# Kernel optimization log

Hardware: AMD Instinct MI355X
Metric: run time of the kernel (lower is better)

The kernel has to match this reference:

```python
import jax, jax.numpy as jnp
import numpy as np

DIMS = [1024, 2048, 2048, 51]
B, P = 16, 1024


def setup_inputs() -> dict:
    key = jax.random.key(0)
    ks = jax.random.split(key, 1 + 2 * (len(DIMS) - 1))
    inp = {
        "num_pairs": P,
        "classifier_input": jax.random.normal(ks[0], (B, P, DIMS[0]), dtype=jnp.float32),
        "num_batches": B,
    }
    # Linear params, PyTorch-style: W[out, in], b[out]
    for li in range(len(DIMS) - 1):
        fan_in = DIMS[li]
        bound = 1.0 / np.sqrt(fan_in)
        inp[f"W{li}"] = jax.random.uniform(ks[1 + 2 * li], (DIMS[li + 1], fan_in), minval=-bound, maxval=bound, dtype=jnp.float32)
        inp[f"b{li}"] = jax.random.uniform(ks[2 + 2 * li], (DIMS[li + 1],), minval=-bound, maxval=bound, dtype=jnp.float32)
    return inp


def reference(num_pairs, classifier_input, num_batches, W0, b0, W1, b1, W2, b2):
    # Batched MLP over all (num_batches * num_pairs) vectors at once.
    # Original loops per (b, i); math is identical. dropout p=0.0 -> identity.
    x = classifier_input  # [B, P, d_in]
    x = jax.nn.relu(jnp.einsum("bpd,hd->bph", x, W0) + b0)
    x = jax.nn.relu(jnp.einsum("bpd,hd->bph", x, W1) + b1)
    out = jnp.einsum("bpd,od->bpo", x, W2) + b2  # [B, P, n_classes]
    return out
```

## Files before the change

### kernel.cpp

```cpp
#include <hip/hip_runtime.h>
#include <hip/hip_bf16.h>
#include <stdint.h>

typedef __attribute__((ext_vector_type(8))) short short8;
typedef __attribute__((ext_vector_type(8))) uint16_t ushort8;
typedef __attribute__((ext_vector_type(4))) float floatx4;

#define TK 64


__device__ __forceinline__ uint16_t f2bf_bits(float f) {
    uint32_t u = __builtin_bit_cast(uint32_t, f);
    u += 0x7FFFu + ((u >> 16) & 1u);
    return (uint16_t)(u >> 16);
}

__device__ __forceinline__ void async_copy16(const void* g, void* l) {
    auto gp = (const __attribute__((address_space(1))) uint32_t*)(uintptr_t)g;
    auto lp = (__attribute__((address_space(3))) uint32_t*)(uint32_t)(uintptr_t)l;
    __builtin_amdgcn_global_load_lds(gp, lp, 16, 0, 0);
}


__global__ void cvt8(const float* __restrict__ src, uint16_t* __restrict__ dst, int n) {
    int i = (blockIdx.x * 256 + threadIdx.x) * 8;
    if (i >= n) return;
    floatx4 a = *(const floatx4*)(src + i);
    floatx4 b = *(const floatx4*)(src + i + 4);
    ushort8 o;
#pragma unroll
    for (int k = 0; k < 4; k++) {
        o[k]     = f2bf_bits(a[k]);
        o[k + 4] = f2bf_bits(b[k]);
    }
    *(ushort8*)(dst + i) = o;
}

__global__ void cvt_pad_w2(const float* __restrict__ src, uint16_t* __restrict__ dst) {
    int i = (blockIdx.x * 256 + threadIdx.x) * 8;
    int row = i >> 11;
    ushort8 o;
    if (row < 51) {
        floatx4 a = *(const floatx4*)(src + i);
        floatx4 b = *(const floatx4*)(src + i + 4);
#pragma unroll
        for (int k = 0; k < 4; k++) {
            o[k]     = f2bf_bits(a[k]);
            o[k + 4] = f2bf_bits(b[k]);
        }
    } else {
#pragma unroll
        for (int k = 0; k < 8; k++) o[k] = 0;
    }
    *(ushort8*)(dst + i) = o;
}


template <int MI, int NJ, bool RELU, bool OUTF32>
__global__ __launch_bounds__(256, 2)
void gemm_bt(const uint16_t* __restrict__ A,
             const uint16_t* __restrict__ W,
             const float* __restrict__ bias,
             void* __restrict__ out,
             int M, int N, int K, int ldc, int nstore)
{
    constexpr int TMv = MI * 32;
    constexpr int TNv = NJ * 32;
    constexpr int ACH = TMv / 32;
    constexpr int BCH = TNv / 32;

    __shared__ alignas(16) uint16_t sA[TMv * TK];
    __shared__ alignas(16) uint16_t sB[TNv * TK];

    const int tid  = threadIdx.x;
    const int wave = tid >> 6;
    const int lane = tid & 63;

    const int f   = blockIdx.x;
    const int xcd = f & 7;
    const int loc = f >> 3;
    const int per = (int)gridDim.x >> 3;
    const int nt  = N / TNv;
    const int n_t = loc % nt;
    const int m_t = xcd * (per / nt) + loc / nt;
    const int n0 = n_t * TNv;
    const int m0 = m_t * TMv;

    floatx4 acc[MI][NJ];
    const floatx4 zero = {0.f, 0.f, 0.f, 0.f};
#pragma unroll
    for (int i = 0; i < MI; i++)
#pragma unroll
        for (int j = 0; j < NJ; j++) acc[i][j] = zero;

    const int wr = (wave >> 1) * MI * 16;
    const int wc = (wave & 1) * NJ * 16;

    const int sr   = lane >> 3;
    const int scol = ((lane & 7) ^ sr) * 8;

    const uint16_t* ap[ACH];
    const uint16_t* bp[BCH];
#pragma unroll
    for (int t = 0; t < ACH; t++)
        ap[t] = A + (size_t)(m0 + (wave + 4 * t) * 8 + sr) * K + scol;
#pragma unroll
    for (int t = 0; t < BCH; t++)
        bp[t] = W + (size_t)(n0 + (wave + 4 * t) * 8 + sr) * K + scol;

    const int fm = lane & 15;
    const int fr = fm & 7;
    const int kgb = lane >> 4;

    const int niter = K / TK;
    for (int it = 0; it < niter; it++) {
#pragma unroll
        for (int t = 0; t < ACH; t++) {
            async_copy16(ap[t], sA + (wave + 4 * t) * 512);
            ap[t] += TK;
        }
#pragma unroll
        for (int t = 0; t < BCH; t++) {
            async_copy16(bp[t], sB + (wave + 4 * t) * 512);
            bp[t] += TK;
        }
        __syncthreads();

#pragma unroll
        for (int kk = 0; kk < 2; kk++) {
            const int slot = ((kgb + 4 * kk) ^ fr) * 8;
            short8 af[MI], bfr[NJ];
#pragma unroll
            for (int i = 0; i < MI; i++)
                af[i] = *(const short8*)(sA + (wr + i * 16 + fm) * TK + slot);
#pragma unroll
            for (int j = 0; j < NJ; j++)
                bfr[j] = *(const short8*)(sB + (wc + j * 16 + fm) * TK + slot);
#pragma unroll
            for (int i = 0; i < MI; i++)
#pragma unroll
                for (int j = 0; j < NJ; j++)
                    acc[i][j] = __builtin_amdgcn_mfma_f32_16x16x32_bf16(af[i], bfr[j], acc[i][j], 0, 0, 0);
        }
        __syncthreads();
    }

    const int cr = (lane >> 4) * 4;
    const int cc = lane & 15;
#pragma unroll
    for (int i = 0; i < MI; i++) {
        const int gmb = m0 + wr + i * 16 + cr;
#pragma unroll
        for (int j = 0; j < NJ; j++) {
            const int gn = n0 + wc + j * 16 + cc;
            if (gn < nstore) {
                const float bv = bias[gn];
#pragma unroll
                for (int r = 0; r < 4; r++) {
                    float v = acc[i][j][r] + bv;
                    if (RELU) v = fmaxf(v, 0.f);
                    const size_t idx = (size_t)(gmb + r) * ldc + gn;
                    if (OUTF32) ((float*)out)[idx] = v;
                    else        ((uint16_t*)out)[idx] = f2bf_bits(v);
                }
            }
        }
    }
}


#define SCHED0 __builtin_amdgcn_sched_barrier(0)

#define LOAD_AF(SA, QM, DST) do { \
    const uint16_t* _p = (SA) + (QM) * 8192 + aoff; \
    _Pragma("unroll") \
    for (int kk = 0; kk < 2; kk++) { \
      const int sl = ((kgb + 4 * kk) ^ fr) * 8; \
      _Pragma("unroll") \
      for (int mi = 0; mi < 4; mi++) \
        DST[mi][kk] = *(const short8*)(_p + mi * 1024 + sl); \
    } } while (0)

#define LOAD_BF(SB, QN, BF) do { \
    const uint16_t* _p = (SB) + (QN) * 8192 + boff; \
    _Pragma("unroll") \
    for (int kk = 0; kk < 2; kk++) { \
      const int sl = ((kgb + 4 * kk) ^ fr) * 8; \
      _Pragma("unroll") \
      for (int nj = 0; nj < 2; nj++) \
        BF[nj][kk] = *(const short8*)(_p + nj * 1024 + sl); \
    } } while (0)

#define PH_SYNC \
    SCHED0; \
    asm volatile("s_waitcnt lgkmcnt(0)" ::: "memory"); \
    SCHED0; \
    __builtin_amdgcn_s_barrier(); \
    SCHED0;

#define PH_SYNC_VM \
    SCHED0; \
    asm volatile("s_waitcnt vmcnt(0) lgkmcnt(0)" ::: "memory"); \
    SCHED0; \
    __builtin_amdgcn_s_barrier(); \
    SCHED0;

#define MFMA_CL(QM, QN, AF, BF) \
    __builtin_amdgcn_s_setprio(1); \
    _Pragma("unroll") \
    for (int kk = 0; kk < 2; kk++) \
      _Pragma("unroll") \
      for (int mi = 0; mi < 4; mi++) \
        _Pragma("unroll") \
        for (int nj = 0; nj < 2; nj++) \
          acc[QM][QN][mi][nj] = __builtin_amdgcn_mfma_f32_16x16x32_bf16( \
              AF[mi][kk], BF[nj][kk], acc[QM][QN][mi][nj], 0, 0, 0); \
    __builtin_amdgcn_s_setprio(0); \
    SCHED0;

#define TILE_BODY(SAc, SBc, SAo, SBo, TT, STG) \
     \
    if (STG) { stB((TT) + 1, SBo); stA((TT) + 1, SAo); } \
    LOAD_AF(SAc, 0, af); \
    LOAD_BF(SBc, 0, b0); \
    LOAD_BF(SBc, 1, b1); \
    PH_SYNC; \
    MFMA_CL(0, 0, af, b0); \
    MFMA_CL(0, 1, af, b1); \
     \
    LOAD_AF(SAc, 1, af); \
    PH_SYNC_VM; \
    MFMA_CL(1, 0, af, b0); \
    MFMA_CL(1, 1, af, b1);

template <bool RELU, bool OUTF32>
__global__ __launch_bounds__(512, 2)
void gemm256(const uint16_t* __restrict__ A,
             const uint16_t* __restrict__ W,
             const float* __restrict__ bias,
             void* __restrict__ out,
             int K, int N, int ldc, int nstore)
{
    extern __shared__ uint16_t smem[];
    uint16_t* sA0 = smem;
    uint16_t* sA1 = smem + 16384;
    uint16_t* sB0 = smem + 32768;
    uint16_t* sB1 = smem + 49152;

    const int tid  = threadIdx.x;
    const int wave = tid >> 6;
    const int lane = tid & 63;
    const int wm2  = wave >> 2;
    const int wn2  = wave & 3;

    const int f   = blockIdx.x;
    const int xcd = f & 7;
    const int loc = f >> 3;
    const int per = (int)gridDim.x >> 3;
    const int ntn = N / 256;
    const int n_t = loc % ntn;
    const int m_t = xcd * (per / ntn) + loc / ntn;
    const int m0 = m_t * 256;
    const int n0 = n_t * 256;

    floatx4 acc[2][2][4][2];
    const floatx4 zero = {0.f, 0.f, 0.f, 0.f};
#pragma unroll
    for (int qm = 0; qm < 2; qm++)
#pragma unroll
    for (int qn = 0; qn < 2; qn++)
#pragma unroll
    for (int mi = 0; mi < 4; mi++)
#pragma unroll
    for (int nj = 0; nj < 2; nj++) acc[qm][qn][mi][nj] = zero;

    const int srow = lane >> 3;
    const int scol = ((lane & 7) ^ srow) * 8;
    const uint16_t* pA = A + (size_t)(m0 + wave * 8 + srow) * K + scol;
    const uint16_t* pB = W + (size_t)(n0 + wave * 8 + srow) * K + scol;

    auto stA = [&](int kt, uint16_t* buf) {
        const uint16_t* p = pA + (size_t)kt * 64;
        async_copy16(p,                    buf + wave * 512);
        async_copy16(p + (size_t)64  * K,  buf + 4096  + wave * 512);
        async_copy16(p + (size_t)128 * K,  buf + 8192  + wave * 512);
        async_copy16(p + (size_t)192 * K,  buf + 12288 + wave * 512);
    };
    auto stB = [&](int kt, uint16_t* buf) {
        const uint16_t* p = pB + (size_t)kt * 64;
        async_copy16(p,                    buf + wave * 512);
        async_copy16(p + (size_t)64  * K,  buf + 4096  + wave * 512);
        async_copy16(p + (size_t)128 * K,  buf + 8192  + wave * 512);
        async_copy16(p + (size_t)192 * K,  buf + 12288 + wave * 512);
    };

    const int fm  = lane & 15;
    const int fr  = fm & 7;
    const int kgb = lane >> 4;
    const int aoff = (wm2 * 64 + fm) * 64;
    const int boff = (wn2 * 32 + fm) * 64;

    short8 af[4][2];
    short8 b0[2][2];
    short8 b1[2][2];

    stB(0, sB0);
    stA(0, sA0);
    asm volatile("s_waitcnt vmcnt(0)" ::: "memory");
    __builtin_amdgcn_s_barrier();
    SCHED0;

    const int niter = K / 64;
    for (int it = 0; it < niter / 2 - 1; ++it) {
        TILE_BODY(sA0, sB0, sA1, sB1, 2 * it,     true);
        TILE_BODY(sA1, sB1, sA0, sB0, 2 * it + 1, true);
    }
    TILE_BODY(sA0, sB0, sA1, sB1, niter - 2, true);
    TILE_BODY(sA1, sB1, sA0, sB0, niter - 1, false);

    const int cr = (lane >> 4) * 4;
    const int cc = lane & 15;
#pragma unroll
    for (int qm = 0; qm < 2; qm++)
#pragma unroll
    for (int mi = 0; mi < 4; mi++) {
        const int gm = m0 + qm * 128 + wm2 * 64 + mi * 16 + cr;
#pragma unroll
        for (int qn = 0; qn < 2; qn++)
#pragma unroll
        for (int nj = 0; nj < 2; nj++) {
            const int gn = n0 + qn * 128 + wn2 * 32 + nj * 16 + cc;
            if (gn < nstore) {
                const float bv = bias[gn];
#pragma unroll
                for (int r = 0; r < 4; r++) {
                    float v = acc[qm][qn][mi][nj][r] + bv;
                    if (RELU) v = fmaxf(v, 0.f);
                    const size_t idx = (size_t)(gm + r) * ldc + gn;
                    if (OUTF32) ((float*)out)[idx] = v;
                    else        ((uint16_t*)out)[idx] = f2bf_bits(v);
                }
            }
        }
    }
}


extern "C" void kernel_launch(void* const* d_in, const int* in_sizes, int n_in,
                              void* d_out, int out_size, void* d_ws, size_t ws_size,
                              hipStream_t stream) {
    (void)in_sizes; (void)n_in; (void)out_size; (void)ws_size;
    const float* X  = (const float*)d_in[1];
    const float* W0 = (const float*)d_in[3];
    const float* b0 = (const float*)d_in[4];
    const float* W1 = (const float*)d_in[5];
    const float* b1 = (const float*)d_in[6];
    const float* W2 = (const float*)d_in[7];
    const float* b2 = (const float*)d_in[8];

    const int M = 16384;

    static bool attr_done = false;
    if (!attr_done) {
        (void)hipFuncSetAttribute((const void*)gemm256<true, false>,
                                  hipFuncAttributeMaxDynamicSharedMemorySize, 131072);
        attr_done = true;
    }

    char* w = (char*)d_ws;
    uint16_t* X0  = (uint16_t*)w; w += (size_t)M * 1024 * 2;
    uint16_t* X1  = (uint16_t*)w; w += (size_t)M * 2048 * 2;
    uint16_t* X2  = (uint16_t*)w; w += (size_t)M * 2048 * 2;
    uint16_t* W0b = (uint16_t*)w; w += (size_t)2048 * 1024 * 2;
    uint16_t* W1b = (uint16_t*)w; w += (size_t)2048 * 2048 * 2;
    uint16_t* W2b = (uint16_t*)w; w += (size_t)64 * 2048 * 2;

    cvt8<<<M * 1024 / 8 / 256, 256, 0, stream>>>(X, X0, M * 1024);
    cvt8<<<2048 * 1024 / 8 / 256, 256, 0, stream>>>(W0, W0b, 2048 * 1024);
    cvt8<<<2048 * 2048 / 8 / 256, 256, 0, stream>>>(W1, W1b, 2048 * 2048);
    cvt_pad_w2<<<64 * 2048 / 8 / 256, 256, 0, stream>>>(W2, W2b);

    gemm256<true, false><<<dim3((M / 256) * (2048 / 256)), 512, 131072, stream>>>(
        X0, W0b, b0, X1, 1024, 2048, 2048, 2048);
    gemm256<true, false><<<dim3((M / 256) * (2048 / 256)), 512, 131072, stream>>>(
        X1, W1b, b1, X2, 2048, 2048, 2048, 2048);
    gemm_bt<1, 2, false, true><<<dim3(M / 32), 256, 0, stream>>>(
        X2, W2b, b2, d_out, M, 64, 2048, 51, 51);
}
```

Baseline: 351.0 us.

## Restructure GEMM barrier schedule and add direct-load small-N final layer kernel

The main 256x256 GEMM loop changes its synchronisation: each phase now issues a barrier before waiting on LDS reads and adds trailing barriers, and the global-load wait moves to the end of the second half-window, so the LDS reads overlap the barrier. The final 51-column layer now uses a new kernel that loads A and W fragments straight from global memory into MFMA registers without LDS staging, replacing the tiled gemm_bt. This trades the LDS tiling for fewer instructions and no block-level syncs in the small-N layer, but it relies on the cache for reuse. The extra barriers in the main loop may also add stall time.

```diff
diff --git a/kernel.cpp b/kernel.cpp
--- a/kernel.cpp
+++ b/kernel.cpp
@@ -169,7 +169,70 @@
 }
 
 
+template <bool RELU, bool OUTF32>
+__global__ __launch_bounds__(256)
+void gemm_small_n(const uint16_t* __restrict__ A,
+                  const uint16_t* __restrict__ W,
+                  const float* __restrict__ bias,
+                  void* __restrict__ out,
+                  int K, int ldc, int nstore)
+{
+    const int tid  = threadIdx.x;
+    const int wave = tid >> 6;
+    const int lane = tid & 63;
+    const int wr = (wave >> 1) * 16;
+    const int wc = (wave & 1) * 32;
+
+    const int m0 = blockIdx.x * 32;
+    const int fm  = lane & 15;
+    const int kgb = lane >> 4;
+
+    const uint16_t* pa  = A + (size_t)(m0 + wr + fm) * K + kgb * 8;
+    const uint16_t* pb0 = W + (size_t)(wc + fm) * K + kgb * 8;
+    const uint16_t* pb1 = W + (size_t)(wc + 16 + fm) * K + kgb * 8;
+
+    floatx4 acc0 = {0.f, 0.f, 0.f, 0.f};
+    floatx4 acc1 = {0.f, 0.f, 0.f, 0.f};
+
+#pragma unroll 8
+    for (int k0 = 0; k0 < K; k0 += 64) {
+#pragma unroll
+        for (int kk = 0; kk < 2; kk++) {
+            const int off = k0 + kk * 32;
+            short8 a  = *(const short8*)(pa  + off);
+            short8 b0 = *(const short8*)(pb0 + off);
+            short8 b1 = *(const short8*)(pb1 + off);
+            acc0 = __builtin_amdgcn_mfma_f32_16x16x32_bf16(a, b0, acc0, 0, 0, 0);
+            acc1 = __builtin_amdgcn_mfma_f32_16x16x32_bf16(a, b1, acc1, 0, 0, 0);
+        }
+    }
+
+    const int cr = (lane >> 4) * 4;
+    const int cc = lane & 15;
+    const int gm = m0 + wr + cr;
+#pragma unroll
+    for (int j = 0; j < 2; j++) {
+        const int gn = wc + j * 16 + cc;
+        if (gn < nstore) {
+            const float bv = bias[gn];
+            const floatx4 av = j ? acc1 : acc0;
+#pragma unroll
+            for (int r = 0; r < 4; r++) {
+                float v = av[r] + bv;
+                if (RELU) v = fmaxf(v, 0.f);
+                const size_t idx = (size_t)(gm + r) * ldc + gn;
+                if (OUTF32) ((float*)out)[idx] = v;
+                else        ((uint16_t*)out)[idx] = f2bf_bits(v);
+            }
+        }
+    }
+}
+
+
 #define SCHED0 __builtin_amdgcn_sched_barrier(0)
+#define BAR    __builtin_amdgcn_s_barrier()
+#define LGKM0  asm volatile("s_waitcnt lgkmcnt(0)" ::: "memory")
+#define VM0    asm volatile("s_waitcnt vmcnt(0)" ::: "memory")
 
 #define LOAD_AF(SA, QM, DST) do { \
     const uint16_t* _p = (SA) + (QM) * 8192 + aoff; \
@@ -190,20 +253,6 @@
       for (int nj = 0; nj < 2; nj++) \
         BF[nj][kk] = *(const short8*)(_p + nj * 1024 + sl); \
     } } while (0)
-
-#define PH_SYNC \
-    SCHED0; \
-    asm volatile("s_waitcnt lgkmcnt(0)" ::: "memory"); \
-    SCHED0; \
-    __builtin_amdgcn_s_barrier(); \
-    SCHED0;
-
-#define PH_SYNC_VM \
-    SCHED0; \
-    asm volatile("s_waitcnt vmcnt(0) lgkmcnt(0)" ::: "memory"); \
-    SCHED0; \
-    __builtin_amdgcn_s_barrier(); \
-    SCHED0;
 
 #define MFMA_CL(QM, QN, AF, BF) \
     __builtin_amdgcn_s_setprio(1); \
@@ -218,20 +267,24 @@
     __builtin_amdgcn_s_setprio(0); \
     SCHED0;
 
-#define TILE_BODY(SAc, SBc, SAo, SBo, TT, STG) \
-     \
+#define WIN_A(SAc, SBc, SAo, SBo, TT, STG) \
     if (STG) { stB((TT) + 1, SBo); stA((TT) + 1, SAo); } \
     LOAD_AF(SAc, 0, af); \
     LOAD_BF(SBc, 0, b0); \
     LOAD_BF(SBc, 1, b1); \
-    PH_SYNC; \
+    SCHED0; BAR; \
+    LGKM0; SCHED0; \
     MFMA_CL(0, 0, af, b0); \
     MFMA_CL(0, 1, af, b1); \
-     \
+    BAR; SCHED0;
+
+#define WIN_B(SAc) \
     LOAD_AF(SAc, 1, af); \
-    PH_SYNC_VM; \
+    SCHED0; BAR; \
+    LGKM0; SCHED0; \
     MFMA_CL(1, 0, af, b0); \
-    MFMA_CL(1, 1, af, b1);
+    MFMA_CL(1, 1, af, b1); \
+    VM0; SCHED0; BAR; SCHED0;
 
 template <bool RELU, bool OUTF32>
 __global__ __launch_bounds__(512, 2)
@@ -306,17 +359,18 @@
 
     stB(0, sB0);
     stA(0, sA0);
-    asm volatile("s_waitcnt vmcnt(0)" ::: "memory");
-    __builtin_amdgcn_s_barrier();
+    VM0;
+    BAR;
     SCHED0;
 
     const int niter = K / 64;
-    for (int it = 0; it < niter / 2 - 1; ++it) {
-        TILE_BODY(sA0, sB0, sA1, sB1, 2 * it,     true);
-        TILE_BODY(sA1, sB1, sA0, sB0, 2 * it + 1, true);
-    }
-    TILE_BODY(sA0, sB0, sA1, sB1, niter - 2, true);
-    TILE_BODY(sA1, sB1, sA0, sB0, niter - 1, false);
+    for (int it = 0; it < niter / 2; ++it) {
+        const int T = 2 * it;
+        WIN_A(sA0, sB0, sA1, sB1, T, true);
+        WIN_B(sA0);
+        WIN_A(sA1, sB1, sA0, sB0, T + 1, T + 2 < niter);
+        WIN_B(sA1);
+    }
 
     const int cr = (lane >> 4) * 4;
     const int cc = lane & 15;
@@ -384,6 +438,6 @@
         X0, W0b, b0, X1, 1024, 2048, 2048, 2048);
     gemm256<true, false><<<dim3((M / 256) * (2048 / 256)), 512, 131072, stream>>>(
         X1, W1b, b1, X2, 2048, 2048, 2048, 2048);
-    gemm_bt<1, 2, false, true><<<dim3(M / 32), 256, 0, stream>>>(
-        X2, W2b, b2, d_out, M, 64, 2048, 51, 51);
-}
+    gemm_small_n<false, true><<<dim3(M / 32), 256, 0, stream>>>(
+        X2, W2b, b2, d_out, 2048, 51, 51);
+}
```

Result: slower. 388.7 us (+10.7%).
